# Optimization experiments

Hardware: AMD Instinct MI355X
Metric: run time of the kernel (lower is better)

The kernel has to match this reference:

```python
import jax, jax.numpy as jnp
import numpy as np

B, N, C = 8, 4096, 1024
H = 16
D = C // H  # head_dim = 64
SCALE = D ** -0.5


def setup_inputs() -> dict:
    key = jax.random.key(0)
    ks = jax.random.split(key, 5)
    std = C ** -0.5
    return {
        "x": jax.random.normal(ks[0], (B, N, C), dtype=jnp.float32),
        "Wq": jax.random.normal(ks[1], (C, C), dtype=jnp.float32) * std,
        "Wk": jax.random.normal(ks[2], (C, C), dtype=jnp.float32) * std,
        "Wv": jax.random.normal(ks[3], (C, C), dtype=jnp.float32) * std,
        "Wo": jax.random.normal(ks[4], (C, C), dtype=jnp.float32) * std,
        "bo": jnp.zeros((C,), dtype=jnp.float32),
    }


def reference(x, Wq, Wk, Wv, Wo, bo):
    b, n, c = x.shape
    # projections -> (B, N, H, D)
    q = (x @ Wq).reshape(b, n, H, D)
    k = (x @ Wk).reshape(b, n, H, D)
    v = (x @ Wv).reshape(b, n, H, D)
    # feature maps: softmax over head_dim for q, over sequence for k
    q = jax.nn.softmax(q, axis=-1) * SCALE
    k = jax.nn.softmax(k, axis=1)
    # O(N) linear attention: kv summary then apply to q
    kv = jnp.einsum("bnhf,bnhd->bhfd", k, v)   # (B, H, D, D)
    y = jnp.einsum("bnhf,bhfd->bnhd", q, kv)   # (B, N, H, D)
    y = y.reshape(b, n, H * D)
    return y @ Wo + bo
```

## Files before the change

kernel.cpp:

```cpp
#include <hip/hip_runtime.h>


typedef unsigned short u16;
typedef __bf16 bf16x8v __attribute__((ext_vector_type(8)));
typedef float f32x4 __attribute__((ext_vector_type(4)));
typedef u16 u16x8 __attribute__((ext_vector_type(8)));
typedef u16 u16x4 __attribute__((ext_vector_type(4)));

#define AS1C(p) (const __attribute__((address_space(1))) void*)(p)
#define AS3(p)  (__attribute__((address_space(3))) void*)(p)

__device__ __forceinline__ float b2f(u16 u) {
    union { unsigned u; float f; } c; c.u = ((unsigned)u) << 16; return c.f;
}
__device__ __forceinline__ u16 f2b(float f) {
    union { float f; unsigned u; } c; c.f = f;
    unsigned x = c.u + 0x7fffu + ((c.u >> 16) & 1u);
    return (u16)(x >> 16);
}

__global__ void prep(const float* __restrict__ x, u16* __restrict__ xb,
                     const float* __restrict__ Wq, const float* __restrict__ Wk,
                     const float* __restrict__ Wv, const float* __restrict__ Wo,
                     u16* __restrict__ wt, u16* __restrict__ wot) {
    if (blockIdx.x < 1024) {
        __shared__ float tl[64][65];
        const int which = blockIdx.x >> 8;
        const float* src = which == 0 ? Wq : which == 1 ? Wk : which == 2 ? Wv : Wo;
        u16* dst = which < 3 ? wt + which * 1048576 : wot;
        const int bx = blockIdx.x & 255;
        const int tx = bx & 15, ty = bx >> 4;
        const int j = threadIdx.x & 63, i0 = threadIdx.x >> 6;
        #pragma unroll
        for (int it = 0; it < 16; ++it) {
            int i = it * 4 + i0;
            tl[i][j] = src[(ty * 64 + i) * 1024 + tx * 64 + j];
        }
        __syncthreads();
        #pragma unroll
        for (int it = 0; it < 16; ++it) {
            int i = it * 4 + i0;
            dst[(tx * 64 + i) * 1024 + ty * 64 + j] = f2b(tl[j][i]);
        }
    } else {
        const long n4 = 8388608L;
        long i = (long)(blockIdx.x - 1024) * blockDim.x + threadIdx.x;
        long stride = 2048L * blockDim.x;
        for (long jj = i; jj < n4; jj += stride) {
            float4 v = ((const float4*)x)[jj];
            u16x4 o = { f2b(v.x), f2b(v.y), f2b(v.z), f2b(v.w) };
            ((u16x4*)xb)[jj] = o;
        }
    }
}

template<int OUTMODE>
__global__ __launch_bounds__(512, 2) void gemm256(
    const u16* __restrict__ A, const u16* __restrict__ Bt,
    void* __restrict__ Cout, const float* __restrict__ bias,
    const int lda, const int ldc, const int ntn, const int nwg, const long btBatch)
{
    __shared__ __align__(16) u16 lds[65536];
    const int t = threadIdx.x;
    const int w = t >> 6, lane = t & 63;
    const int l16 = lane & 15, g = lane >> 4;
    const int wr = w >> 2, wc = w & 3;

    const int cpx = nwg >> 3;
    const int bid = blockIdx.x;
    const int swzb = (bid & 7) * cpx + (bid >> 3);
    const int tm = swzb / ntn, tn = swzb - tm * ntn;
    const long row0 = (long)tm << 8, col0 = (long)tn << 8;
    const u16* BtB = Bt + (row0 >> 12) * btBatch;

    const int eo = (((t & 7) ^ ((t >> 3) & 7)) << 3);
    const u16* pA = A + (row0 + (t >> 3)) * (long)lda + eo;
    const u16* pB = BtB + (col0 + (t >> 3)) * 1024L + eo;
    const long a64 = (long)lda << 6;

#define STG_A(Tt, j) __builtin_amdgcn_global_load_lds(                        \
    AS1C(pA + (long)(j) * a64 + (((Tt) & 15) << 6)),                          \
    AS3(lds + ((((Tt) & 1) << 15) + ((j) << 12) + t * 8)), 16, 0, 0);
#define STG_B(Tt, j) __builtin_amdgcn_global_load_lds(                        \
    AS1C(pB + (long)(j) * 65536L + (((Tt) & 15) << 6)),                       \
    AS3(lds + ((((Tt) & 1) << 15) + 16384 + ((j) << 12) + t * 8)), 16, 0, 0);

    const int swz = l16 & 7;
    const int koff0 = ((0 * 4 + g) ^ swz) << 3;
    const int koff1 = ((1 * 4 + g) ^ swz) << 3;
    const int arow = ((wr << 7) + l16) << 6;
    const int brow = 16384 + (((wc << 6) + l16) << 6);

    u16x8 aM[4][2], b0[2][2], b1[2][2];
    f32x4 acc[8][4] = {};

#define RD_A(half) { _Pragma("unroll") for (int mi = 0; mi < 4; ++mi) {       \
    const int ab = bufE + arow + ((half) * 64 + mi * 16) * 64;                \
    aM[mi][0] = *(const u16x8*)&lds[ab + koff0];                              \
    aM[mi][1] = *(const u16x8*)&lds[ab + koff1]; } }
#define RD_B(nh, br) { _Pragma("unroll") for (int ni = 0; ni < 2; ++ni) {     \
    const int bb = bufE + brow + ((nh) * 32 + ni * 16) * 64;                  \
    br[ni][0] = *(const u16x8*)&lds[bb + koff0];                              \
    br[ni][1] = *(const u16x8*)&lds[bb + koff1]; } }
#define MM(mh, nh, br) { __builtin_amdgcn_s_setprio(1);                       \
    _Pragma("unroll") for (int mi = 0; mi < 4; ++mi)                          \
    { _Pragma("unroll") for (int ni = 0; ni < 2; ++ni) {                      \
    f32x4 c = acc[(mh)*4 + mi][(nh)*2 + ni];                                  \
    c = __builtin_amdgcn_mfma_f32_16x16x32_bf16(                              \
        __builtin_bit_cast(bf16x8v, aM[mi][0]),                               \
        __builtin_bit_cast(bf16x8v, br[ni][0]), c, 0, 0, 0);                  \
    c = __builtin_amdgcn_mfma_f32_16x16x32_bf16(                              \
        __builtin_bit_cast(bf16x8v, aM[mi][1]),                               \
        __builtin_bit_cast(bf16x8v, br[ni][1]), c, 0, 0, 0);                  \
    acc[(mh)*4 + mi][(nh)*2 + ni] = c; } }                                    \
    __builtin_amdgcn_s_setprio(0); }

    STG_A(0, 0) STG_A(0, 2) STG_B(0, 0) STG_B(0, 1)
    STG_B(0, 2) STG_B(0, 3) STG_A(0, 1) STG_A(0, 3)
    STG_A(1, 0) STG_A(1, 2) STG_B(1, 0) STG_B(1, 1)
    asm volatile("s_waitcnt vmcnt(6)" ::: "memory");
    __builtin_amdgcn_s_barrier();

    #pragma unroll 2
    for (int T = 0; T < 16; ++T) {
        const int bufE = (T & 1) << 15;
        RD_A(0) RD_B(0, b0)
        STG_B(T + 1, 2) STG_B(T + 1, 3)
        __builtin_amdgcn_s_barrier();
        MM(0, 0, b0)
        RD_B(1, b1)
        STG_A(T + 1, 1) STG_A(T + 1, 3)
        asm volatile("s_waitcnt vmcnt(8)" ::: "memory");
        __builtin_amdgcn_s_barrier();
        MM(0, 1, b1)
        RD_A(1)
        STG_A(T + 2, 0) STG_A(T + 2, 2)
        __builtin_amdgcn_s_barrier();
        MM(1, 0, b0)
        STG_B(T + 2, 0) STG_B(T + 2, 1)
        asm volatile("s_waitcnt vmcnt(6)" ::: "memory");
        __builtin_amdgcn_s_barrier();
        MM(1, 1, b1)
    }
    asm volatile("s_waitcnt vmcnt(0)" ::: "memory");
#undef STG_A
#undef STG_B
#undef RD_A
#undef RD_B
#undef MM

    if (OUTMODE == 2 && tn < 4) {
        #pragma unroll
        for (int mi = 0; mi < 8; ++mi) {
            #pragma unroll
            for (int r = 0; r < 4; ++r) {
                float v0 = acc[mi][0][r], v1 = acc[mi][1][r];
                float v2 = acc[mi][2][r], v3 = acc[mi][3][r];
                float m = fmaxf(fmaxf(v0, v1), fmaxf(v2, v3));
                m = fmaxf(m, __shfl_xor(m, 1)); m = fmaxf(m, __shfl_xor(m, 2));
                m = fmaxf(m, __shfl_xor(m, 4)); m = fmaxf(m, __shfl_xor(m, 8));
                v0 = __expf(v0 - m); v1 = __expf(v1 - m);
                v2 = __expf(v2 - m); v3 = __expf(v3 - m);
                float s = v0 + v1 + v2 + v3;
                s += __shfl_xor(s, 1); s += __shfl_xor(s, 2);
                s += __shfl_xor(s, 4); s += __shfl_xor(s, 8);
                const float sc = 0.125f / s;
                acc[mi][0][r] = v0 * sc; acc[mi][1][r] = v1 * sc;
                acc[mi][2][r] = v2 * sc; acc[mi][3][r] = v3 * sc;
            }
        }
    }
    if (OUTMODE == 2 && tn >= 4 && tn < 8) {
        #pragma unroll
        for (int mi = 0; mi < 8; ++mi)
            #pragma unroll
            for (int ni = 0; ni < 4; ++ni)
                #pragma unroll
                for (int r = 0; r < 4; ++r)
                    acc[mi][ni][r] = __expf(acc[mi][ni][r]);
    }

    const long crow = row0 + wr * 128 + g * 4;
    const long ccol = col0 + wc * 64 + l16;
    if (OUTMODE != 1) {
        u16* Cb = (u16*)Cout;
        #pragma unroll
        for (int mi = 0; mi < 8; ++mi) {
            #pragma unroll
            for (int ni = 0; ni < 4; ++ni) {
                long base = (crow + mi * 16) * (long)ldc + ccol + ni * 16;
                #pragma unroll
                for (int r = 0; r < 4; ++r)
                    Cb[base + (long)r * ldc] = f2b(acc[mi][ni][r]);
            }
        }
    } else {
        float* Cf = (float*)Cout;
        float bv[4];
        #pragma unroll
        for (int ni = 0; ni < 4; ++ni) bv[ni] = bias[ccol + ni * 16];
        #pragma unroll
        for (int mi = 0; mi < 8; ++mi) {
            #pragma unroll
            for (int ni = 0; ni < 4; ++ni) {
                long base = (crow + mi * 16) * (long)ldc + ccol + ni * 16;
                #pragma unroll
                for (int r = 0; r < 4; ++r)
                    Cf[base + (long)r * ldc] = acc[mi][ni][r] + bv[ni];
            }
        }
    }
}

__global__ __launch_bounds__(256) void kv_partial(const u16* __restrict__ qkv,
                                                  float* __restrict__ kvp,
                                                  float* __restrict__ psum) {
    __shared__ __align__(16) float kf_s[64 * 68];
    __shared__ __align__(16) float v_s[64 * 68];
    const int t = threadIdx.x;
    const int bx = blockIdx.x;
    const int nc = bx & 7, h = (bx >> 3) & 15, b = bx >> 7;
    const int f0 = (t >> 4) << 2;
    const int d0 = (t & 15) << 2;
    const int lr = t >> 3, lc = (t & 7) << 3;
    const long rowbase = (long)b * 4096 + nc * 512;
    const u16* kfg = qkv + (rowbase + lr) * 3072 + 1024 + h * 64 + lc;
    const u16* vg = kfg + 1024;
    float acc[4][4] = {};
    float cs[4] = {};
    for (int n0 = 0; n0 < 512; n0 += 64) {
        long go = (long)n0 * 3072;
        u16x8 kr0 = *(const u16x8*)(kfg + go);
        u16x8 kr1 = *(const u16x8*)(kfg + go + 32L * 3072);
        u16x8 vr0 = *(const u16x8*)(vg + go);
        u16x8 vr1 = *(const u16x8*)(vg + go + 32L * 3072);
        f32x4 ke0a, ke0b, ke1a, ke1b, vv0a, vv0b, vv1a, vv1b;
        #pragma unroll
        for (int j = 0; j < 4; ++j) {
            ke0a[j] = b2f(kr0[j]);     ke0b[j] = b2f(kr0[j + 4]);
            ke1a[j] = b2f(kr1[j]);     ke1b[j] = b2f(kr1[j + 4]);
            vv0a[j] = b2f(vr0[j]);     vv0b[j] = b2f(vr0[j + 4]);
            vv1a[j] = b2f(vr1[j]);     vv1b[j] = b2f(vr1[j + 4]);
        }
        *(f32x4*)&kf_s[lr * 68 + lc]            = ke0a;
        *(f32x4*)&kf_s[lr * 68 + lc + 4]        = ke0b;
        *(f32x4*)&kf_s[(lr + 32) * 68 + lc]     = ke1a;
        *(f32x4*)&kf_s[(lr + 32) * 68 + lc + 4] = ke1b;
        *(f32x4*)&v_s[lr * 68 + lc]             = vv0a;
        *(f32x4*)&v_s[lr * 68 + lc + 4]         = vv0b;
        *(f32x4*)&v_s[(lr + 32) * 68 + lc]      = vv1a;
        *(f32x4*)&v_s[(lr + 32) * 68 + lc + 4]  = vv1b;
        __syncthreads();
        #pragma unroll 8
        for (int r = 0; r < 64; ++r) {
            f32x4 kf4 = *(const f32x4*)&kf_s[r * 68 + f0];
            f32x4 vf4 = *(const f32x4*)&v_s[r * 68 + d0];
            #pragma unroll
            for (int i = 0; i < 4; ++i) {
                cs[i] += kf4[i];
                #pragma unroll
                for (int jj = 0; jj < 4; ++jj)
                    acc[i][jj] += kf4[i] * vf4[jj];
            }
        }
        __syncthreads();
    }
    float* o = kvp + (long)nc * 524288 + ((long)(b * 16 + h)) * 4096;
    #pragma unroll
    for (int i = 0; i < 4; ++i) {
        #pragma unroll
        for (int jj = 0; jj < 4; ++jj)
            o[(f0 + i) * 64 + d0 + jj] = acc[i][jj];
    }
    if ((t & 15) == 0) {
        float* ps = psum + ((long)nc * 128 + b * 16 + h) * 64 + f0;
        #pragma unroll
        for (int i = 0; i < 4; ++i) ps[i] = cs[i];
    }
}

__global__ void kv_scale(const float* __restrict__ kvp, const float* __restrict__ psum,
                         u16* __restrict__ kvNb) {
    __shared__ float inv_s[64];
    const int bh = blockIdx.x;
    const int t = threadIdx.x;
    if (t < 64) {
        float s = 0.f;
        #pragma unroll
        for (int nc = 0; nc < 8; ++nc) s += psum[((long)nc * 128 + bh) * 64 + t];
        inv_s[t] = 1.0f / s;
    }
    __syncthreads();
    const float* p = kvp + (long)bh * 4096;
    u16* o = kvNb + (long)bh * 4096;
    const float inv = inv_s[t >> 2];
    #pragma unroll
    for (int j = 0; j < 4; ++j) {
        const int idx = t * 16 + j * 4;
        f32x4 v = {};
        #pragma unroll
        for (int nc = 0; nc < 8; ++nc) {
            f32x4 pv = *(const f32x4*)&p[(long)nc * 524288 + idx];
            #pragma unroll
            for (int e = 0; e < 4; ++e) v[e] += pv[e];
        }
        u16x4 ov = { f2b(v[0] * inv), f2b(v[1] * inv), f2b(v[2] * inv), f2b(v[3] * inv) };
        *(u16x4*)&o[idx] = ov;
    }
}

__global__ __launch_bounds__(256) void w2t_mfma(const u16* __restrict__ wot,
                                                const u16* __restrict__ kvNb,
                                                u16* __restrict__ w2t) {
    __shared__ __align__(16) u16 Qs[8192];
    const int t = threadIdx.x;
    const int bx = blockIdx.x;
    const int mt = bx & 7, h = (bx >> 3) & 15, b = bx >> 7;
    const int c0 = mt * 128;
    const int wave = t >> 6, lane = t & 63;
    const int wr = wave >> 1, wc = wave & 1;
    const int l16 = lane & 15, g = lane >> 4;

    const int colg = t & 7;
    const int rloc = t >> 3;
    #pragma unroll
    for (int p = 0; p < 4; ++p) {
        const int row = p * 32 + rloc;
        u16x8 qv = *(const u16x8*)(wot + (long)(c0 + row) * 1024 + h * 64 + colg * 8);
        const int chunk = colg ^ (row & 7);
        *(u16x8*)&Qs[row * 64 + chunk * 8] = qv;
    }
    __syncthreads();

    const u16* kvb = kvNb + ((long)(b * 16 + h) << 12);
    bf16x8v bkv[2][2];
    #pragma unroll
    for (int ni = 0; ni < 2; ++ni) {
        #pragma unroll
        for (int ks = 0; ks < 2; ++ks)
            bkv[ni][ks] = __builtin_bit_cast(bf16x8v,
                *(const u16x8*)(kvb + (wc * 32 + ni * 16 + l16) * 64 + ks * 32 + g * 8));
    }
    bf16x8v aq[4][2];
    #pragma unroll
    for (int mi = 0; mi < 4; ++mi) {
        const int row = wr * 64 + mi * 16 + l16;
        #pragma unroll
        for (int ks = 0; ks < 2; ++ks) {
            const int c16 = (ks * 4 + g) ^ (row & 7);
            aq[mi][ks] = __builtin_bit_cast(bf16x8v,
                *(const u16x8*)&Qs[row * 64 + c16 * 8]);
        }
    }
    f32x4 acc[4][2] = {};
    #pragma unroll
    for (int mi = 0; mi < 4; ++mi) {
        #pragma unroll
        for (int ni = 0; ni < 2; ++ni) {
            acc[mi][ni] = __builtin_amdgcn_mfma_f32_16x16x32_bf16(
                aq[mi][0], bkv[ni][0], acc[mi][ni], 0, 0, 0);
            acc[mi][ni] = __builtin_amdgcn_mfma_f32_16x16x32_bf16(
                aq[mi][1], bkv[ni][1], acc[mi][ni], 0, 0, 0);
        }
    }
    u16* ob = w2t + (long)b * 1048576;
    #pragma unroll
    for (int mi = 0; mi < 4; ++mi) {
        #pragma unroll
        for (int ni = 0; ni < 2; ++ni) {
            int row = c0 + wr * 64 + mi * 16 + g * 4;
            int col = h * 64 + wc * 32 + ni * 16 + l16;
            #pragma unroll
            for (int r = 0; r < 4; ++r)
                ob[(long)(row + r) * 1024 + col] = f2b(acc[mi][ni][r]);
        }
    }
}

extern "C" void kernel_launch(void* const* d_in, const int* in_sizes, int n_in,
                              void* d_out, int out_size, void* d_ws, size_t ws_size,
                              hipStream_t stream) {
    (void)in_sizes; (void)n_in; (void)out_size; (void)ws_size;
    const float* x  = (const float*)d_in[0];
    const float* Wq = (const float*)d_in[1];
    const float* Wk = (const float*)d_in[2];
    const float* Wv = (const float*)d_in[3];
    const float* Wo = (const float*)d_in[4];
    const float* bo = (const float*)d_in[5];

    u16* xb  = (u16*)d_ws;
    u16* wt  = xb + 33554432;
    u16* wot = wt + 3145728;
    u16* qkv = wot + 1048576;
    u16* kvNb = qkv + 100663296;
    float* kvp  = (float*)xb;
    float* psum = kvp + 4194304;
    u16* w2t = (u16*)(psum + 65536);

    prep<<<3072, 256, 0, stream>>>(x, xb, Wq, Wk, Wv, Wo, wt, wot);
    gemm256<2><<<1536, 512, 0, stream>>>(xb, wt, (void*)qkv, nullptr, 1024, 3072, 12, 1536, 0L);
    kv_partial<<<1024, 256, 0, stream>>>(qkv, kvp, psum);
    kv_scale<<<128, 256, 0, stream>>>(kvp, psum, kvNb);
    w2t_mfma<<<1024, 256, 0, stream>>>(wot, kvNb, w2t);
    gemm256<1><<<512, 512, 0, stream>>>(qkv, w2t, d_out, bo, 3072, 1024, 4, 512, 1048576L);
}
```

Before: 385.4 us.

## Compute KV partial outer products with bf16 MFMA and swizzled transposed LDS

```diff
diff --git a/kernel.cpp b/kernel.cpp
--- a/kernel.cpp
+++ b/kernel.cpp
@@ -212,70 +212,84 @@
     }
 }
 
-__global__ __launch_bounds__(256) void kv_partial(const u16* __restrict__ qkv,
-                                                  float* __restrict__ kvp,
-                                                  float* __restrict__ psum) {
-    __shared__ __align__(16) float kf_s[64 * 68];
-    __shared__ __align__(16) float v_s[64 * 68];
+__global__ __launch_bounds__(256) void kv_mfma(const u16* __restrict__ qkv,
+                                               float* __restrict__ kvp,
+                                               float* __restrict__ psum) {
+    __shared__ __align__(16) u16 eT[64 * 72];
+    __shared__ __align__(16) u16 vT[64 * 72];
+    __shared__ float csb[256 * 8];
     const int t = threadIdx.x;
     const int bx = blockIdx.x;
     const int nc = bx & 7, h = (bx >> 3) & 15, b = bx >> 7;
-    const int f0 = (t >> 4) << 2;
-    const int d0 = (t & 15) << 2;
-    const int lr = t >> 3, lc = (t & 7) << 3;
+    const int r = t >> 3;
+    const int c = t & 7;
     const long rowbase = (long)b * 4096 + nc * 512;
-    const u16* kfg = qkv + (rowbase + lr) * 3072 + 1024 + h * 64 + lc;
-    const u16* vg = kfg + 1024;
-    float acc[4][4] = {};
-    float cs[4] = {};
+    const u16* eg = qkv + (rowbase + r) * 3072 + 1024 + h * 64 + c * 8;
+    const u16* vg = eg + 1024;
+    const int w = t >> 6, lane = t & 63;
+    const int l16 = lane & 15, g = lane >> 4;
+
+    float cs[8] = {};
+    f32x4 acc[4] = {};
+
+    int aoff[2], boff[4][2];
+    #pragma unroll
+    for (int ks = 0; ks < 2; ++ks) {
+        const int f = w * 16 + l16;
+        aoff[ks] = f * 72 + ((ks * 32 + g * 8) ^ (((f >> 3) & 7) << 3));
+        #pragma unroll
+        for (int db = 0; db < 4; ++db) {
+            const int d = db * 16 + l16;
+            boff[db][ks] = d * 72 + ((ks * 32 + g * 8) ^ (((d >> 3) & 7) << 3));
+        }
+    }
+
     for (int n0 = 0; n0 < 512; n0 += 64) {
-        long go = (long)n0 * 3072;
-        u16x8 kr0 = *(const u16x8*)(kfg + go);
-        u16x8 kr1 = *(const u16x8*)(kfg + go + 32L * 3072);
-        u16x8 vr0 = *(const u16x8*)(vg + go);
-        u16x8 vr1 = *(const u16x8*)(vg + go + 32L * 3072);
-        f32x4 ke0a, ke0b, ke1a, ke1b, vv0a, vv0b, vv1a, vv1b;
-        #pragma unroll
-        for (int j = 0; j < 4; ++j) {
-            ke0a[j] = b2f(kr0[j]);     ke0b[j] = b2f(kr0[j + 4]);
-            ke1a[j] = b2f(kr1[j]);     ke1b[j] = b2f(kr1[j + 4]);
-            vv0a[j] = b2f(vr0[j]);     vv0b[j] = b2f(vr0[j + 4]);
-            vv1a[j] = b2f(vr1[j]);     vv1b[j] = b2f(vr1[j + 4]);
-        }
-        *(f32x4*)&kf_s[lr * 68 + lc]            = ke0a;
-        *(f32x4*)&kf_s[lr * 68 + lc + 4]        = ke0b;
-        *(f32x4*)&kf_s[(lr + 32) * 68 + lc]     = ke1a;
-        *(f32x4*)&kf_s[(lr + 32) * 68 + lc + 4] = ke1b;
-        *(f32x4*)&v_s[lr * 68 + lc]             = vv0a;
-        *(f32x4*)&v_s[lr * 68 + lc + 4]         = vv0b;
-        *(f32x4*)&v_s[(lr + 32) * 68 + lc]      = vv1a;
-        *(f32x4*)&v_s[(lr + 32) * 68 + lc + 4]  = vv1b;
+        const long go = (long)n0 * 3072;
+        u16x8 e0 = *(const u16x8*)(eg + go);
+        u16x8 e1 = *(const u16x8*)(eg + go + 32L * 3072);
+        u16x8 v0 = *(const u16x8*)(vg + go);
+        u16x8 v1 = *(const u16x8*)(vg + go + 32L * 3072);
+        #pragma unroll
+        for (int j = 0; j < 8; ++j) {
+            cs[j] += b2f(e0[j]) + b2f(e1[j]);
+            const int f = c * 8 + j;
+            const int sw = ((f >> 3) & 7) << 3;
+            eT[f * 72 + (r ^ sw)]        = e0[j];
+            eT[f * 72 + ((r + 32) ^ sw)] = e1[j];
+            vT[f * 72 + (r ^ sw)]        = v0[j];
+            vT[f * 72 + ((r + 32) ^ sw)] = v1[j];
+        }
         __syncthreads();
+        #pragma unroll
+        for (int ks = 0; ks < 2; ++ks) {
+            bf16x8v af = __builtin_bit_cast(bf16x8v, *(const u16x8*)&eT[aoff[ks]]);
+            #pragma unroll
+            for (int db = 0; db < 4; ++db) {
+                bf16x8v bf = __builtin_bit_cast(bf16x8v, *(const u16x8*)&vT[boff[db][ks]]);
+                acc[db] = __builtin_amdgcn_mfma_f32_16x16x32_bf16(af, bf, acc[db], 0, 0, 0);
+            }
+        }
+        __syncthreads();
+    }
+
+    float* o = kvp + (long)nc * 524288 + ((long)(b * 16 + h)) * 4096;
+    #pragma unroll
+    for (int db = 0; db < 4; ++db) {
+        #pragma unroll
+        for (int rr = 0; rr < 4; ++rr)
+            o[(w * 16 + g * 4 + rr) * 64 + db * 16 + l16] = acc[db][rr];
+    }
+
+    #pragma unroll
+    for (int j = 0; j < 8; ++j) csb[t * 8 + j] = cs[j];
+    __syncthreads();
+    if (t < 64) {
+        const int cc = t >> 3, jj = t & 7;
+        float s = 0.f;
         #pragma unroll 8
-        for (int r = 0; r < 64; ++r) {
-            f32x4 kf4 = *(const f32x4*)&kf_s[r * 68 + f0];
-            f32x4 vf4 = *(const f32x4*)&v_s[r * 68 + d0];
-            #pragma unroll
-            for (int i = 0; i < 4; ++i) {
-                cs[i] += kf4[i];
-                #pragma unroll
-                for (int jj = 0; jj < 4; ++jj)
-                    acc[i][jj] += kf4[i] * vf4[jj];
-            }
-        }
-        __syncthreads();
-    }
-    float* o = kvp + (long)nc * 524288 + ((long)(b * 16 + h)) * 4096;
-    #pragma unroll
-    for (int i = 0; i < 4; ++i) {
-        #pragma unroll
-        for (int jj = 0; jj < 4; ++jj)
-            o[(f0 + i) * 64 + d0 + jj] = acc[i][jj];
-    }
-    if ((t & 15) == 0) {
-        float* ps = psum + ((long)nc * 128 + b * 16 + h) * 64 + f0;
-        #pragma unroll
-        for (int i = 0; i < 4; ++i) ps[i] = cs[i];
+        for (int rr = 0; rr < 32; ++rr) s += csb[(cc + 8 * rr) * 8 + jj];
+        psum[((long)nc * 128 + b * 16 + h) * 64 + t] = s;
     }
 }
 
@@ -399,7 +413,7 @@
 
     prep<<<3072, 256, 0, stream>>>(x, xb, Wq, Wk, Wv, Wo, wt, wot);
     gemm256<2><<<1536, 512, 0, stream>>>(xb, wt, (void*)qkv, nullptr, 1024, 3072, 12, 1536, 0L);
-    kv_partial<<<1024, 256, 0, stream>>>(qkv, kvp, psum);
+    kv_mfma<<<1024, 256, 0, stream>>>(qkv, kvp, psum);
     kv_scale<<<128, 256, 0, stream>>>(kvp, psum, kvNb);
     w2t_mfma<<<1024, 256, 0, stream>>>(wot, kvNb, w2t);
     gemm256<1><<<512, 512, 0, stream>>>(qkv, w2t, d_out, bo, 3072, 1024, 4, 512, 1048576L);
```

New measurement: 356.1 us. 1.08x faster.
